# Kernel optimization log

Hardware: AMD Instinct MI355X
Metric: run time of the kernel (lower is better)

The kernel has to match this reference:

```python
import jax, jax.numpy as jnp
import numpy as np
import math

D_MODEL = 512
NUM_HEADS = 8
HEAD_DIM = D_MODEL // NUM_HEADS
B, L = 2, 2048
LN_EPS = 1e-5
DEN_EPS = 1e-5


def setup_inputs() -> dict:
    key = jax.random.key(0)
    ks = jax.random.split(key, 6)
    s = 1.0 / math.sqrt(D_MODEL)
    return {
        "x": jax.random.normal(ks[0], (B, L, D_MODEL), dtype=jnp.float32),
        "Wqkv": jax.random.normal(ks[1], (D_MODEL, 3 * D_MODEL), dtype=jnp.float32) * s,
        "bqkv": jnp.zeros((3 * D_MODEL,), dtype=jnp.float32),
        "Wout": jax.random.normal(ks[2], (D_MODEL, D_MODEL), dtype=jnp.float32) * s,
        "bout": jnp.zeros((D_MODEL,), dtype=jnp.float32),
        "ln_gamma": jnp.ones((D_MODEL,), dtype=jnp.float32),
        "ln_beta": jnp.zeros((D_MODEL,), dtype=jnp.float32),
        "decay_logits": jnp.full((NUM_HEADS,), 5.0, dtype=jnp.float32),
    }


def reference(x, Wqkv, bqkv, Wout, bout, ln_gamma, ln_beta, decay_logits):
    Bv, Lv, D = x.shape
    H = decay_logits.shape[0]
    E = D // H

    qkv = x @ Wqkv + bqkv                                   # [B,L,3D]
    q, k, v = jnp.split(qkv, 3, axis=-1)
    q = q.reshape(Bv, Lv, H, E)
    k = k.reshape(Bv, Lv, H, E)
    v = v.reshape(Bv, Lv, H, E)

    # ELU feature map + 1 -> positive features; scale q by 1/sqrt(E)
    q = (jax.nn.elu(q) + 1.0) / jnp.sqrt(jnp.asarray(E, x.dtype))
    k = jax.nn.elu(k) + 1.0

    lambdas = jax.nn.sigmoid(decay_logits).reshape(1, 1, H, 1)   # [1,1,H,1]
    t = jnp.arange(Lv, dtype=x.dtype).reshape(1, Lv, 1, 1)       # [1,L,1,1]
    decay_k = jnp.power(lambdas, -t)   # lambda^{-t}
    decay_q = jnp.power(lambdas, t)    # lambda^{t}

    k_dec = k * decay_k                                          # [B,L,H,E]
    kv = jnp.einsum('blhe,blhf->blhef', k_dec, v)                # [B,L,H,E,E]
    memory = jnp.cumsum(kv, axis=1)                              # prefix-sum scan over L
    k_sum = jnp.cumsum(k_dec, axis=1)                            # [B,L,H,E]

    q_dec = q * decay_q
    num = jnp.einsum('blhe,blhef->blhf', q_dec, memory)          # [B,L,H,E]
    den = jnp.einsum('blhe,blhe->blh', q_dec, k_sum)[..., None] + DEN_EPS
    out = (num / den).reshape(Bv, Lv, D)

    out = out @ Wout + bout

    # LayerNorm (eval mode; dropout is identity)
    mu = jnp.mean(out, axis=-1, keepdims=True)
    var = jnp.var(out, axis=-1, keepdims=True)
    out = (out - mu) / jnp.sqrt(var + LN_EPS) * ln_gamma + ln_beta
    return out
```

## Files before the change

kernel.cpp:

```cpp
#include <hip/hip_runtime.h>
#include <math.h>

#define B_ 2
#define L_ 2048
#define D_ 512
#define H_ 8
#define E_ 64
#define CHUNK 32
#define NCH 64
#define DEN_EPS_ 1e-5f
#define LN_EPS_ 1e-5f

typedef __bf16 bf16x8 __attribute__((ext_vector_type(8)));
typedef __bf16 bf16x4 __attribute__((ext_vector_type(4)));
typedef float  f32x4  __attribute__((ext_vector_type(4)));

__device__ __forceinline__ float sigm(float x) { return 1.f / (1.f + expf(-x)); }
__device__ __forceinline__ float elu1(float x) { return x > 0.f ? x + 1.f : expf(x); }

__global__ __launch_bounds__(256) void k_transpose_both(
    const float* __restrict__ W1, __bf16* __restrict__ D1,
    const float* __restrict__ W2, __bf16* __restrict__ D2)
{
    const float* src; __bf16* dst; int N;
    if (blockIdx.z == 0) { src = W1; dst = D1; N = 1536; }
    else                 { if (blockIdx.x >= 8) return; src = W2; dst = D2; N = 512; }
    const int K = 512;

    __shared__ __bf16 tile[64][68];
    const int kb = blockIdx.y * 64, nb = blockIdx.x * 64;
    const int t = threadIdx.x;
    const int rr = t >> 4, cc4 = (t & 15) * 4;
#pragma unroll
    for (int p = 0; p < 4; p++) {
        int k = rr + p * 16;
        float4 v = *(const float4*)&src[(size_t)(kb + k) * N + nb + cc4];
        tile[k][cc4 + 0] = (__bf16)v.x;
        tile[k][cc4 + 1] = (__bf16)v.y;
        tile[k][cc4 + 2] = (__bf16)v.z;
        tile[k][cc4 + 3] = (__bf16)v.w;
    }
    __syncthreads();
#pragma unroll
    for (int p = 0; p < 4; p++) {
        int n = rr + p * 16;
        bf16x4 o;
        o[0] = tile[cc4 + 0][n];
        o[1] = tile[cc4 + 1][n];
        o[2] = tile[cc4 + 2][n];
        o[3] = tile[cc4 + 3][n];
        *(bf16x4*)&dst[(size_t)(nb + n) * K + kb + cc4] = o;
    }
}

__global__ __launch_bounds__(256) void k_mfma_qkv(
    const float* __restrict__ X, const __bf16* __restrict__ Bt,
    const float* __restrict__ bias,
    __bf16* __restrict__ Qb, __bf16* __restrict__ Kb, __bf16* __restrict__ Vb)
{
    __shared__ __bf16 Al[128 * 32];
    __shared__ __bf16 Bl[128 * 32];
    const int t = threadIdx.x;
    const int w = t >> 6, lane = t & 63;
    const int wm = w >> 1, wn = w & 1;
    const int ll = lane & 15, quad = lane >> 4;
    const int m0 = blockIdx.y * 128, n0 = blockIdx.x * 128;

    f32x4 acc[4][4] = {};
    const int sr = t >> 2, sk = (t & 3) * 8;

    float4 pa0[2], pa1[2];
    bf16x8 pb[2];
    auto fetch = [&](int k0) {
#pragma unroll
        for (int h2 = 0; h2 < 2; h2++) {
            const float* ap = X + (size_t)(m0 + sr + h2 * 64) * D_ + k0 + sk;
            pa0[h2] = *(const float4*)ap;
            pa1[h2] = *(const float4*)(ap + 4);
        }
        pb[0] = *(const bf16x8*)&Bt[(size_t)(n0 + sr) * D_ + k0 + sk];
        pb[1] = *(const bf16x8*)&Bt[(size_t)(n0 + sr + 64) * D_ + k0 + sk];
    };

    fetch(0);
    for (int k0 = 0; k0 < D_; k0 += 32) {
#pragma unroll
        for (int h2 = 0; h2 < 2; h2++) {
            bf16x8 o;
            o[0] = (__bf16)pa0[h2].x; o[1] = (__bf16)pa0[h2].y;
            o[2] = (__bf16)pa0[h2].z; o[3] = (__bf16)pa0[h2].w;
            o[4] = (__bf16)pa1[h2].x; o[5] = (__bf16)pa1[h2].y;
            o[6] = (__bf16)pa1[h2].z; o[7] = (__bf16)pa1[h2].w;
            *(bf16x8*)&Al[(sr + h2 * 64) * 32 + sk] = o;
        }
        *(bf16x8*)&Bl[sr * 32 + sk]        = pb[0];
        *(bf16x8*)&Bl[(sr + 64) * 32 + sk] = pb[1];
        __syncthreads();
        if (k0 + 32 < D_) fetch(k0 + 32);
#pragma unroll
        for (int im = 0; im < 4; im++) {
            bf16x8 a = *(const bf16x8*)&Al[(wm * 64 + im * 16 + ll) * 32 + quad * 8];
#pragma unroll
            for (int in = 0; in < 4; in++) {
                bf16x8 b = *(const bf16x8*)&Bl[(wn * 64 + in * 16 + ll) * 32 + quad * 8];
                acc[im][in] = __builtin_amdgcn_mfma_f32_16x16x32_bf16(a, b, acc[im][in], 0, 0, 0);
            }
        }
        __syncthreads();
    }

    const int sec = n0 >> 9;
    __bf16* base = (sec == 0 ? Qb : (sec == 1 ? Kb : Vb));
#pragma unroll
    for (int im = 0; im < 4; im++) {
#pragma unroll
        for (int in = 0; in < 4; in++) {
            int n = n0 + wn * 64 + in * 16 + ll;
            int d = n & 511, h = d >> 6, e = d & 63;
            float bv = bias[n];
#pragma unroll
            for (int r = 0; r < 4; r++) {
                int m = m0 + wm * 64 + im * 16 + quad * 4 + r;
                int bb = m >> 11, l = m & 2047;
                float v = acc[im][in][r] + bv;
                if (sec == 0)      v = elu1(v) * 0.125f;
                else if (sec == 1) v = elu1(v);
                base[((size_t)((bb * H_ + h) * L_ + l)) * E_ + e] = (__bf16)v;
            }
        }
    }
}

__global__ __launch_bounds__(256) void k_chunk_g(
    const __bf16* __restrict__ Kb, const __bf16* __restrict__ Vb,
    const float* __restrict__ dl,
    __bf16* __restrict__ Gt, float* __restrict__ gn)
{
    __shared__ __bf16 Kwt[64][40];
    __shared__ __bf16 Vt[64][40];
    const int t  = threadIdx.x;
    const int bx = blockIdx.x;
    const int n = bx & 63, h = (bx >> 6) & 7, bb = bx >> 9;
    const int bh = bb * H_ + h;
    const float lam = sigm(dl[h]);

    {
        int i = t & 31, e0 = (t >> 5) * 8;
        size_t src = ((size_t)bh * L_ + n * CHUNK + i) * E_ + e0;
        float wk = powf(lam, (float)(CHUNK - 1 - i));
        bf16x8 k8 = *(const bf16x8*)&Kb[src];
        bf16x8 v8 = *(const bf16x8*)&Vb[src];
#pragma unroll
        for (int q = 0; q < 8; q++) {
            Kwt[e0 + q][i] = (__bf16)((float)k8[q] * wk);
            Vt[e0 + q][i]  = v8[q];
        }
    }
    __syncthreads();

    const int w = t >> 6, lane = t & 63;
    const int wm = w >> 1, wn = w & 1;
    const int ll = lane & 15, quad = lane >> 4;

    bf16x8 af[2], bf_[2];
#pragma unroll
    for (int a = 0; a < 2; a++) {
        af[a]  = *(const bf16x8*)&Vt[wm * 32 + a * 16 + ll][quad * 8];
        bf_[a] = *(const bf16x8*)&Kwt[wn * 32 + a * 16 + ll][quad * 8];
    }
    f32x4 acc[2][2] = {};
#pragma unroll
    for (int a = 0; a < 2; a++)
#pragma unroll
        for (int b = 0; b < 2; b++)
            acc[a][b] = __builtin_amdgcn_mfma_f32_16x16x32_bf16(af[a], bf_[b], acc[a][b], 0, 0, 0);

    size_t gbase = ((size_t)bh * NCH + n) * 4096;
#pragma unroll
    for (int a = 0; a < 2; a++)
#pragma unroll
        for (int b = 0; b < 2; b++)
#pragma unroll
            for (int r = 0; r < 4; r++) {
                int f = wm * 32 + a * 16 + quad * 4 + r;
                int e = wn * 32 + b * 16 + ll;
                Gt[gbase + (size_t)f * 64 + e] = (__bf16)acc[a][b][r];
            }

    if (t < 64) {
        float ga = 0.f;
#pragma unroll
        for (int k8 = 0; k8 < 4; k8++) {
            bf16x8 kk = *(const bf16x8*)&Kwt[t][k8 * 8];
#pragma unroll
            for (int q = 0; q < 8; q++) ga += (float)kk[q];
        }
        gn[((size_t)bh * NCH + n) * E_ + t] = ga;
    }
}

__global__ __launch_bounds__(64) void k_scan_par(
    const __bf16* __restrict__ Gt, const float* __restrict__ gn,
    const float* __restrict__ dl,
    __bf16* __restrict__ Sb, float* __restrict__ zl)
{
    const int lane = threadIdx.x;
    const int bh = blockIdx.x >> 6;
    const int j  = blockIdx.x & 63;
    const float lam = sigm(dl[bh & 7]);
    const float dC  = powf(lam, (float)CHUNK);

    const size_t base = ((size_t)bh * NCH) * 4096 + (size_t)j * 64 + lane;

    __bf16 g[NCH];
#pragma unroll
    for (int n = 0; n < NCH; n++) g[n] = Gt[base + (size_t)n * 4096];

    float s = 0.f;
#pragma unroll
    for (int n = 0; n < NCH; n++) {
        Sb[base + (size_t)n * 4096] = (__bf16)(lam * s);
        s = fmaf(dC, s, (float)g[n]);
    }

    float gv = gn[((size_t)bh * NCH + lane) * E_ + j];
    float wf = dC;
#pragma unroll
    for (int k = 1; k < 64; k <<= 1) {
        float up = __shfl_up(gv, k);
        if (lane >= k) gv = fmaf(wf, up, gv);
        wf = wf * wf;
    }
    float zex = __shfl_up(gv, 1);
    if (lane == 0) zex = 0.f;
    zl[((size_t)bh * NCH + lane) * E_ + j] = lam * zex;
}

__global__ __launch_bounds__(256) void k_attn(
    const __bf16* __restrict__ Qb, const __bf16* __restrict__ Kb,
    const __bf16* __restrict__ Vb,
    const __bf16* __restrict__ Sb, const float* __restrict__ zl,
    const float* __restrict__ dl, __bf16* __restrict__ Out)
{
    __shared__ __bf16 Qw[32][64];
    __shared__ __bf16 Kw[32][64];
    __shared__ __bf16 Vt[64][40];
    __shared__ __bf16 SbT[64][72];
    __shared__ __bf16 A1[32][40];
    __shared__ float  den[32];
    __shared__ float  zz[64];

    const int t  = threadIdx.x;
    const int bx = blockIdx.x;
    const int n = bx & 63, h = (bx >> 6) & 7, bb = bx >> 9;
    const int bh = bb * H_ + h;
    const float lam = sigm(dl[h]);

    {
        int i = t >> 3, e0 = (t & 7) * 8;
        size_t src = ((size_t)bh * L_ + n * CHUNK + i) * E_ + e0;
        float wq = powf(lam, (float)i);
        float wk = powf(lam, -(float)i);
        bf16x8 q8 = *(const bf16x8*)&Qb[src];
        bf16x8 k8 = *(const bf16x8*)&Kb[src];
        bf16x8 v8 = *(const bf16x8*)&Vb[src];
        bf16x8 qo, ko;
#pragma unroll
        for (int q = 0; q < 8; q++) {
            qo[q] = (__bf16)((float)q8[q] * wq);
            ko[q] = (__bf16)((float)k8[q] * wk);
            Vt[e0 + q][i] = v8[q];
        }
        *(bf16x8*)&Qw[i][e0] = qo;
        *(bf16x8*)&Kw[i][e0] = ko;

        int f = t >> 2, e00 = (t & 3) * 16;
        size_t sbase = ((size_t)bh * NCH + n) * 4096;
        bf16x8 s0 = *(const bf16x8*)&Sb[sbase + (size_t)f * 64 + e00];
        bf16x8 s1 = *(const bf16x8*)&Sb[sbase + (size_t)f * 64 + e00 + 8];
        *(bf16x8*)&SbT[f][e00]     = s0;
        *(bf16x8*)&SbT[f][e00 + 8] = s1;
        if (t < 64) zz[t] = zl[((size_t)bh * NCH + n) * E_ + t];
    }
    __syncthreads();

    const int w = t >> 6, lane = t & 63;
    const int ll = lane & 15, quad = lane >> 4;

    {
        const int wm = w >> 1, wn = w & 1;
        f32x4 accA = {};
#pragma unroll
        for (int ks = 0; ks < 2; ks++) {
            bf16x8 a = *(const bf16x8*)&Qw[wm * 16 + ll][ks * 32 + quad * 8];
            bf16x8 b = *(const bf16x8*)&Kw[wn * 16 + ll][ks * 32 + quad * 8];
            accA = __builtin_amdgcn_mfma_f32_16x16x32_bf16(a, b, accA, 0, 0, 0);
        }
        int j = wn * 16 + ll;
#pragma unroll
        for (int r = 0; r < 4; r++) {
            int i = wm * 16 + quad * 4 + r;
            A1[i][j] = (__bf16)(j <= i ? accA[r] : 0.f);
        }
    }
    __syncthreads();

    if (t < 32) {
        float rs = 0.f;
#pragma unroll
        for (int k8 = 0; k8 < 4; k8++) {
            bf16x8 aa = *(const bf16x8*)&A1[t][k8 * 8];
#pragma unroll
            for (int q = 0; q < 8; q++) rs += (float)aa[q];
        }
        float qz = 0.f;
#pragma unroll
        for (int e8 = 0; e8 < 8; e8++) {
            bf16x8 qq = *(const bf16x8*)&Qw[t][e8 * 8];
#pragma unroll
            for (int q = 0; q < 8; q++) qz += (float)qq[q] * zz[e8 * 8 + q];
        }
        den[t] = rs + qz + DEN_EPS_;
    }

    const int fw = w * 16;
    f32x4 acc1[2] = {}, acc2[2] = {};
    {
        bf16x8 bV = *(const bf16x8*)&Vt[fw + ll][quad * 8];
#pragma unroll
        for (int im = 0; im < 2; im++) {
            bf16x8 aA = *(const bf16x8*)&A1[im * 16 + ll][quad * 8];
            acc1[im] = __builtin_amdgcn_mfma_f32_16x16x32_bf16(aA, bV, acc1[im], 0, 0, 0);
        }
#pragma unroll
        for (int ks = 0; ks < 2; ks++) {
            bf16x8 bS = *(const bf16x8*)&SbT[fw + ll][ks * 32 + quad * 8];
#pragma unroll
            for (int im = 0; im < 2; im++) {
                bf16x8 aQ = *(const bf16x8*)&Qw[im * 16 + ll][ks * 32 + quad * 8];
                acc2[im] = __builtin_amdgcn_mfma_f32_16x16x32_bf16(aQ, bS, acc2[im], 0, 0, 0);
            }
        }
    }
    __syncthreads();

#pragma unroll
    for (int im = 0; im < 2; im++)
#pragma unroll
        for (int r = 0; r < 4; r++) {
            int i = im * 16 + quad * 4 + r;
            float o = (acc1[im][r] + acc2[im][r]) / den[i];
            Out[((size_t)bb * L_ + n * CHUNK + i) * D_ + h * E_ + fw + ll] = (__bf16)o;
        }
}

__global__ __launch_bounds__(256) void k_mfma_out_ln(
    const __bf16* __restrict__ Ab, const __bf16* __restrict__ Bt,
    const float* __restrict__ bias, const float* __restrict__ gam,
    const float* __restrict__ bet, float* __restrict__ Y)
{
    __shared__ __bf16 Al[32 * 32];
    __shared__ __bf16 Bl[512 * 32];
    __shared__ float gaml[512], betl[512], bl[512];
    __shared__ float redS[4][32], redQ[4][32];
    __shared__ float mv[32][2];

    const int t = threadIdx.x;
    const int w = t >> 6, lane = t & 63;
    const int ll = lane & 15, quad = lane >> 4;
    const int m0 = blockIdx.x * 32;

    {
        float2 g = *(const float2*)&gam[t * 2];
        float2 b2 = *(const float2*)&bet[t * 2];
        float2 bo = *(const float2*)&bias[t * 2];
        gaml[t * 2] = g.x;  gaml[t * 2 + 1] = g.y;
        betl[t * 2] = b2.x; betl[t * 2 + 1] = b2.y;
        bl[t * 2]   = bo.x; bl[t * 2 + 1]   = bo.y;
    }

    f32x4 acc[2][8] = {};
    const int sr = t >> 2, sk = (t & 3) * 8;

    bf16x8 pA;
    bf16x8 pB[8];
    auto fetch = [&](int k0) {
        if (t < 128)
            pA = *(const bf16x8*)&Ab[(size_t)(m0 + sr) * D_ + k0 + sk];
#pragma unroll
        for (int p = 0; p < 8; p++)
            pB[p] = *(const bf16x8*)&Bt[(size_t)(sr + p * 64) * D_ + k0 + sk];
    };

    fetch(0);
    for (int k0 = 0; k0 < D_; k0 += 32) {
        if (t < 128)
            *(bf16x8*)&Al[sr * 32 + sk] = pA;
#pragma unroll
        for (int p = 0; p < 8; p++)
            *(bf16x8*)&Bl[(sr + p * 64) * 32 + sk] = pB[p];
        __syncthreads();
        if (k0 + 32 < D_) fetch(k0 + 32);
#pragma unroll
        for (int im = 0; im < 2; im++) {
            bf16x8 a = *(const bf16x8*)&Al[(im * 16 + ll) * 32 + quad * 8];
#pragma unroll
            for (int in = 0; in < 8; in++) {
                bf16x8 b = *(const bf16x8*)&Bl[(w * 128 + in * 16 + ll) * 32 + quad * 8];
                acc[im][in] = __builtin_amdgcn_mfma_f32_16x16x32_bf16(a, b, acc[im][in], 0, 0, 0);
            }
        }
        __syncthreads();
    }

    float vals[2][8][4];
    float ps[2][4] = {}, pq[2][4] = {};
#pragma unroll
    for (int im = 0; im < 2; im++)
#pragma unroll
        for (int in = 0; in < 8; in++) {
            int col = w * 128 + in * 16 + ll;
            float bv = bl[col];
#pragma unroll
            for (int r = 0; r < 4; r++) {
                float v = acc[im][in][r] + bv;
                vals[im][in][r] = v;
                ps[im][r] += v;
                pq[im][r] += v * v;
            }
        }
#pragma unroll
    for (int im = 0; im < 2; im++)
#pragma unroll
        for (int r = 0; r < 4; r++) {
            float s = ps[im][r], q = pq[im][r];
            s += __shfl_xor(s, 1); q += __shfl_xor(q, 1);
            s += __shfl_xor(s, 2); q += __shfl_xor(q, 2);
            s += __shfl_xor(s, 4); q += __shfl_xor(q, 4);
            s += __shfl_xor(s, 8); q += __shfl_xor(q, 8);
            if (ll == 0) {
                int row = im * 16 + quad * 4 + r;
                redS[w][row] = s;
                redQ[w][row] = q;
            }
        }
    __syncthreads();
    if (t < 32) {
        float S = redS[0][t] + redS[1][t] + redS[2][t] + redS[3][t];
        float Q = redQ[0][t] + redQ[1][t] + redQ[2][t] + redQ[3][t];
        float mu  = S * (1.f / 512.f);
        float var = Q * (1.f / 512.f) - mu * mu;
        mv[t][0] = mu;
        mv[t][1] = rsqrtf(var + LN_EPS_);
    }
    __syncthreads();
#pragma unroll
    for (int im = 0; im < 2; im++)
#pragma unroll
        for (int r = 0; r < 4; r++) {
            int row = im * 16 + quad * 4 + r;
            float mu = mv[row][0], rs = mv[row][1];
#pragma unroll
            for (int in = 0; in < 8; in++) {
                int col = w * 128 + in * 16 + ll;
                Y[(size_t)(m0 + row) * D_ + col] =
                    (vals[im][in][r] - mu) * rs * gaml[col] + betl[col];
            }
        }
}

extern "C" void kernel_launch(void* const* d_in, const int* in_sizes, int n_in,
                              void* d_out, int out_size, void* d_ws, size_t ws_size,
                              hipStream_t stream)
{
    const float* x    = (const float*)d_in[0];
    const float* Wqkv = (const float*)d_in[1];
    const float* bqkv = (const float*)d_in[2];
    const float* Wout = (const float*)d_in[3];
    const float* bout = (const float*)d_in[4];
    const float* gam  = (const float*)d_in[5];
    const float* bet  = (const float*)d_in[6];
    const float* dl   = (const float*)d_in[7];
    float* out = (float*)d_out;

    const size_t NBHLE = (size_t)B_ * H_ * L_ * E_;
    const size_t NG    = (size_t)B_ * H_ * NCH * E_ * E_;
    const size_t Ng    = (size_t)B_ * H_ * NCH * E_;

    char* p = (char*)d_ws;
    __bf16* Gt  = (__bf16*)p;    p += NG * 2;
    __bf16* Sb  = (__bf16*)p;    p += NG * 2;
    float*  gn  = (float*)p;     p += Ng * 4;
    float*  zl  = (float*)p;     p += Ng * 4;
    __bf16* Qb  = (__bf16*)p;    p += NBHLE * 2;
    __bf16* Kb  = (__bf16*)p;    p += NBHLE * 2;
    __bf16* Vb  = (__bf16*)p;    p += NBHLE * 2;
    __bf16* WqkvT = (__bf16*)p;  p += (size_t)1536 * 512 * 2;
    __bf16* WoutT = (__bf16*)p;  p += (size_t)512 * 512 * 2;
    __bf16* Ao    = (__bf16*)p;  p += NBHLE * 2;

    dim3 blk(256);
    k_transpose_both<<<dim3(24, 8, 2), blk, 0, stream>>>(Wqkv, WqkvT, Wout, WoutT);
    k_mfma_qkv      <<<dim3(12, 32),   blk, 0, stream>>>(x, WqkvT, bqkv, Qb, Kb, Vb);
    k_chunk_g       <<<dim3(1024),     blk, 0, stream>>>(Kb, Vb, dl, Gt, gn);
    k_scan_par      <<<dim3(1024),     dim3(64), 0, stream>>>(Gt, gn, dl, Sb, zl);
    k_attn          <<<dim3(1024),     blk, 0, stream>>>(Qb, Kb, Vb, Sb, zl, dl, Ao);
    k_mfma_out_ln   <<<dim3(128),      blk, 0, stream>>>(Ao, WoutT, bout, gam, bet, out);
}
```

Measured before the change: 131.4 us.

## Use async global-to-LDS loads with swizzled LDS in GEMMs, pre-convert X to bf16

X is converted to bf16 in a prep kernel that also transposes the weights. Both GEMMs now stage tiles with global_load_lds direct copies into XOR-swizzled LDS instead of register prefetch plus ds_write. The attention kernel reads the state matrix straight into registers rather than through an LDS transpose, and swizzles the Q/K tiles to reduce bank conflicts. In exchange the GEMMs lose their register double-buffer prefetch, so load latency is no longer overlapped with MFMA work, and the X conversion costs an extra pass over memory.

```diff
diff --git a/kernel.cpp b/kernel.cpp
--- a/kernel.cpp
+++ b/kernel.cpp
@@ -18,18 +18,41 @@
 __device__ __forceinline__ float sigm(float x) { return 1.f / (1.f + expf(-x)); }
 __device__ __forceinline__ float elu1(float x) { return x > 0.f ? x + 1.f : expf(x); }
 
-__global__ __launch_bounds__(256) void k_transpose_both(
+__device__ __forceinline__ void async_cp16(const void* g, void* l) {
+    __builtin_amdgcn_global_load_lds(
+        (const __attribute__((address_space(1))) void*)g,
+        (__attribute__((address_space(3))) void*)l, 16, 0, 0);
+}
+
+#define SWZ4(row, q) ((((q) ^ ((row) & 3)) * 8))
+
+__global__ __launch_bounds__(256) void k_prep(
     const float* __restrict__ W1, __bf16* __restrict__ D1,
-    const float* __restrict__ W2, __bf16* __restrict__ D2)
-{
+    const float* __restrict__ W2, __bf16* __restrict__ D2,
+    const float* __restrict__ X,  __bf16* __restrict__ Xb)
+{
+    const int t = threadIdx.x;
+    if (blockIdx.z == 2) {
+        int id = ((int)blockIdx.y * 32 + (int)blockIdx.x) * 256 + t;
+#pragma unroll
+        for (int it = 0; it < 4; it++) {
+            size_t i = (size_t)it * 524288 + (size_t)id * 8;
+            float4 a = *(const float4*)&X[i];
+            float4 b = *(const float4*)&X[i + 4];
+            bf16x8 o;
+            o[0] = (__bf16)a.x; o[1] = (__bf16)a.y; o[2] = (__bf16)a.z; o[3] = (__bf16)a.w;
+            o[4] = (__bf16)b.x; o[5] = (__bf16)b.y; o[6] = (__bf16)b.z; o[7] = (__bf16)b.w;
+            *(bf16x8*)&Xb[i] = o;
+        }
+        return;
+    }
     const float* src; __bf16* dst; int N;
-    if (blockIdx.z == 0) { src = W1; dst = D1; N = 1536; }
-    else                 { if (blockIdx.x >= 8) return; src = W2; dst = D2; N = 512; }
+    if (blockIdx.z == 0) { if (blockIdx.x >= 24) return; src = W1; dst = D1; N = 1536; }
+    else                 { if (blockIdx.x >= 8)  return; src = W2; dst = D2; N = 512; }
     const int K = 512;
 
     __shared__ __bf16 tile[64][68];
     const int kb = blockIdx.y * 64, nb = blockIdx.x * 64;
-    const int t = threadIdx.x;
     const int rr = t >> 4, cc4 = (t & 15) * 4;
 #pragma unroll
     for (int p = 0; p < 4; p++) {
@@ -54,7 +77,7 @@
 }
 
 __global__ __launch_bounds__(256) void k_mfma_qkv(
-    const float* __restrict__ X, const __bf16* __restrict__ Bt,
+    const __bf16* __restrict__ Ab, const __bf16* __restrict__ Bt,
     const float* __restrict__ bias,
     __bf16* __restrict__ Qb, __bf16* __restrict__ Kb, __bf16* __restrict__ Vb)
 {
@@ -67,42 +90,28 @@
     const int m0 = blockIdx.y * 128, n0 = blockIdx.x * 128;
 
     f32x4 acc[4][4] = {};
-    const int sr = t >> 2, sk = (t & 3) * 8;
-
-    float4 pa0[2], pa1[2];
-    bf16x8 pb[2];
-    auto fetch = [&](int k0) {
-#pragma unroll
-        for (int h2 = 0; h2 < 2; h2++) {
-            const float* ap = X + (size_t)(m0 + sr + h2 * 64) * D_ + k0 + sk;
-            pa0[h2] = *(const float4*)ap;
-            pa1[h2] = *(const float4*)(ap + 4);
-        }
-        pb[0] = *(const bf16x8*)&Bt[(size_t)(n0 + sr) * D_ + k0 + sk];
-        pb[1] = *(const bf16x8*)&Bt[(size_t)(n0 + sr + 64) * D_ + k0 + sk];
-    };
-
-    fetch(0);
+    const int sr  = t >> 2;
+    const int skz = (((t & 3) ^ (sr & 3)) * 8);
+
+    __bf16* A0 = &Al[(w * 16) * 32];
+    __bf16* A1p = &Al[(64 + w * 16) * 32];
+    __bf16* B0 = &Bl[(w * 16) * 32];
+    __bf16* B1p = &Bl[(64 + w * 16) * 32];
+
     for (int k0 = 0; k0 < D_; k0 += 32) {
-#pragma unroll
-        for (int h2 = 0; h2 < 2; h2++) {
-            bf16x8 o;
-            o[0] = (__bf16)pa0[h2].x; o[1] = (__bf16)pa0[h2].y;
-            o[2] = (__bf16)pa0[h2].z; o[3] = (__bf16)pa0[h2].w;
-            o[4] = (__bf16)pa1[h2].x; o[5] = (__bf16)pa1[h2].y;
-            o[6] = (__bf16)pa1[h2].z; o[7] = (__bf16)pa1[h2].w;
-            *(bf16x8*)&Al[(sr + h2 * 64) * 32 + sk] = o;
-        }
-        *(bf16x8*)&Bl[sr * 32 + sk]        = pb[0];
-        *(bf16x8*)&Bl[(sr + 64) * 32 + sk] = pb[1];
+        async_cp16(&Ab[(size_t)(m0 + sr) * D_ + k0 + skz],      A0);
+        async_cp16(&Ab[(size_t)(m0 + 64 + sr) * D_ + k0 + skz], A1p);
+        async_cp16(&Bt[(size_t)(n0 + sr) * D_ + k0 + skz],      B0);
+        async_cp16(&Bt[(size_t)(n0 + 64 + sr) * D_ + k0 + skz], B1p);
         __syncthreads();
-        if (k0 + 32 < D_) fetch(k0 + 32);
 #pragma unroll
         for (int im = 0; im < 4; im++) {
-            bf16x8 a = *(const bf16x8*)&Al[(wm * 64 + im * 16 + ll) * 32 + quad * 8];
+            int ra = wm * 64 + im * 16 + ll;
+            bf16x8 a = *(const bf16x8*)&Al[ra * 32 + SWZ4(ra, quad)];
 #pragma unroll
             for (int in = 0; in < 4; in++) {
-                bf16x8 b = *(const bf16x8*)&Bl[(wn * 64 + in * 16 + ll) * 32 + quad * 8];
+                int rb = wn * 64 + in * 16 + ll;
+                bf16x8 b = *(const bf16x8*)&Bl[rb * 32 + SWZ4(rb, quad)];
                 acc[im][in] = __builtin_amdgcn_mfma_f32_16x16x32_bf16(a, b, acc[im][in], 0, 0, 0);
             }
         }
@@ -245,7 +254,6 @@
     __shared__ __bf16 Qw[32][64];
     __shared__ __bf16 Kw[32][64];
     __shared__ __bf16 Vt[64][40];
-    __shared__ __bf16 SbT[64][72];
     __shared__ __bf16 A1[32][40];
     __shared__ float  den[32];
     __shared__ float  zz[64];
@@ -256,44 +264,45 @@
     const int bh = bb * H_ + h;
     const float lam = sigm(dl[h]);
 
+    const int w = t >> 6, lane = t & 63;
+    const int ll = lane & 15, quad = lane >> 4;
+    const int fw = w * 16;
+    const size_t sbase = ((size_t)bh * NCH + n) * 4096;
+
+    bf16x8 bS0 = *(const bf16x8*)&Sb[sbase + (size_t)(fw + ll) * 64 + quad * 8];
+    bf16x8 bS1 = *(const bf16x8*)&Sb[sbase + (size_t)(fw + ll) * 64 + 32 + quad * 8];
+
     {
-        int i = t >> 3, e0 = (t & 7) * 8;
-        size_t src = ((size_t)bh * L_ + n * CHUNK + i) * E_ + e0;
+        int i = t >> 3, e0c = t & 7;
+        size_t src = ((size_t)bh * L_ + n * CHUNK + i) * E_ + e0c * 8;
         float wq = powf(lam, (float)i);
         float wk = powf(lam, -(float)i);
         bf16x8 q8 = *(const bf16x8*)&Qb[src];
         bf16x8 k8 = *(const bf16x8*)&Kb[src];
         bf16x8 v8 = *(const bf16x8*)&Vb[src];
         bf16x8 qo, ko;
+        int e0 = e0c * 8;
 #pragma unroll
         for (int q = 0; q < 8; q++) {
             qo[q] = (__bf16)((float)q8[q] * wq);
             ko[q] = (__bf16)((float)k8[q] * wk);
             Vt[e0 + q][i] = v8[q];
         }
-        *(bf16x8*)&Qw[i][e0] = qo;
-        *(bf16x8*)&Kw[i][e0] = ko;
-
-        int f = t >> 2, e00 = (t & 3) * 16;
-        size_t sbase = ((size_t)bh * NCH + n) * 4096;
-        bf16x8 s0 = *(const bf16x8*)&Sb[sbase + (size_t)f * 64 + e00];
-        bf16x8 s1 = *(const bf16x8*)&Sb[sbase + (size_t)f * 64 + e00 + 8];
-        *(bf16x8*)&SbT[f][e00]     = s0;
-        *(bf16x8*)&SbT[f][e00 + 8] = s1;
+        int cs = (e0c ^ (i & 7)) * 8;
+        *(bf16x8*)&Qw[i][cs] = qo;
+        *(bf16x8*)&Kw[i][cs] = ko;
         if (t < 64) zz[t] = zl[((size_t)bh * NCH + n) * E_ + t];
     }
     __syncthreads();
-
-    const int w = t >> 6, lane = t & 63;
-    const int ll = lane & 15, quad = lane >> 4;
 
     {
         const int wm = w >> 1, wn = w & 1;
+        int ra = wm * 16 + ll, rb = wn * 16 + ll;
         f32x4 accA = {};
 #pragma unroll
         for (int ks = 0; ks < 2; ks++) {
-            bf16x8 a = *(const bf16x8*)&Qw[wm * 16 + ll][ks * 32 + quad * 8];
-            bf16x8 b = *(const bf16x8*)&Kw[wn * 16 + ll][ks * 32 + quad * 8];
+            bf16x8 a = *(const bf16x8*)&Qw[ra][((ks * 4 + quad) ^ (ra & 7)) * 8];
+            bf16x8 b = *(const bf16x8*)&Kw[rb][((ks * 4 + quad) ^ (rb & 7)) * 8];
             accA = __builtin_amdgcn_mfma_f32_16x16x32_bf16(a, b, accA, 0, 0, 0);
         }
         int j = wn * 16 + ll;
@@ -316,14 +325,13 @@
         float qz = 0.f;
 #pragma unroll
         for (int e8 = 0; e8 < 8; e8++) {
-            bf16x8 qq = *(const bf16x8*)&Qw[t][e8 * 8];
-#pragma unroll
-            for (int q = 0; q < 8; q++) qz += (float)qq[q] * zz[e8 * 8 + q];
+            bf16x8 qq = *(const bf16x8*)&Qw[t][(e8 ^ (t & 7)) * 8];
+#pragma unroll
+            for (int q = 0; q < 8; q++) qz += (float)qq[q] * zz[(e8 ^ (t & 7)) * 8 + q];
         }
         den[t] = rs + qz + DEN_EPS_;
     }
 
-    const int fw = w * 16;
     f32x4 acc1[2] = {}, acc2[2] = {};
     {
         bf16x8 bV = *(const bf16x8*)&Vt[fw + ll][quad * 8];
@@ -333,13 +341,12 @@
             acc1[im] = __builtin_amdgcn_mfma_f32_16x16x32_bf16(aA, bV, acc1[im], 0, 0, 0);
         }
 #pragma unroll
-        for (int ks = 0; ks < 2; ks++) {
-            bf16x8 bS = *(const bf16x8*)&SbT[fw + ll][ks * 32 + quad * 8];
-#pragma unroll
-            for (int im = 0; im < 2; im++) {
-                bf16x8 aQ = *(const bf16x8*)&Qw[im * 16 + ll][ks * 32 + quad * 8];
-                acc2[im] = __builtin_amdgcn_mfma_f32_16x16x32_bf16(aQ, bS, acc2[im], 0, 0, 0);
-            }
+        for (int im = 0; im < 2; im++) {
+            int ra = im * 16 + ll;
+            bf16x8 aQ0 = *(const bf16x8*)&Qw[ra][((quad) ^ (ra & 7)) * 8];
+            bf16x8 aQ1 = *(const bf16x8*)&Qw[ra][((4 + quad) ^ (ra & 7)) * 8];
+            acc2[im] = __builtin_amdgcn_mfma_f32_16x16x32_bf16(aQ0, bS0, acc2[im], 0, 0, 0);
+            acc2[im] = __builtin_amdgcn_mfma_f32_16x16x32_bf16(aQ1, bS1, acc2[im], 0, 0, 0);
         }
     }
     __syncthreads();
@@ -380,33 +387,25 @@
     }
 
     f32x4 acc[2][8] = {};
-    const int sr = t >> 2, sk = (t & 3) * 8;
-
-    bf16x8 pA;
-    bf16x8 pB[8];
-    auto fetch = [&](int k0) {
-        if (t < 128)
-            pA = *(const bf16x8*)&Ab[(size_t)(m0 + sr) * D_ + k0 + sk];
-#pragma unroll
-        for (int p = 0; p < 8; p++)
-            pB[p] = *(const bf16x8*)&Bt[(size_t)(sr + p * 64) * D_ + k0 + sk];
-    };
-
-    fetch(0);
+    const int sr  = t >> 2;
+    const int skz = (((t & 3) ^ (sr & 3)) * 8);
+    __bf16* Ald = &Al[(w * 16) * 32];
+
     for (int k0 = 0; k0 < D_; k0 += 32) {
         if (t < 128)
-            *(bf16x8*)&Al[sr * 32 + sk] = pA;
+            async_cp16(&Ab[(size_t)(m0 + sr) * D_ + k0 + skz], Ald);
 #pragma unroll
         for (int p = 0; p < 8; p++)
-            *(bf16x8*)&Bl[(sr + p * 64) * 32 + sk] = pB[p];
+            async_cp16(&Bt[(size_t)(p * 64 + sr) * D_ + k0 + skz], &Bl[(p * 64 + w * 16) * 32]);
         __syncthreads();
-        if (k0 + 32 < D_) fetch(k0 + 32);
 #pragma unroll
         for (int im = 0; im < 2; im++) {
-            bf16x8 a = *(const bf16x8*)&Al[(im * 16 + ll) * 32 + quad * 8];
+            int ra = im * 16 + ll;
+            bf16x8 a = *(const bf16x8*)&Al[ra * 32 + SWZ4(ra, quad)];
 #pragma unroll
             for (int in = 0; in < 8; in++) {
-                bf16x8 b = *(const bf16x8*)&Bl[(w * 128 + in * 16 + ll) * 32 + quad * 8];
+                int rb = w * 128 + in * 16 + ll;
+                bf16x8 b = *(const bf16x8*)&Bl[rb * 32 + SWZ4(rb, quad)];
                 acc[im][in] = __builtin_amdgcn_mfma_f32_16x16x32_bf16(a, b, acc[im][in], 0, 0, 0);
             }
         }
@@ -495,15 +494,16 @@
     __bf16* Qb  = (__bf16*)p;    p += NBHLE * 2;
     __bf16* Kb  = (__bf16*)p;    p += NBHLE * 2;
     __bf16* Vb  = (__bf16*)p;    p += NBHLE * 2;
+    __bf16* Xb    = (__bf16*)p;  p += NBHLE * 2;
     __bf16* WqkvT = (__bf16*)p;  p += (size_t)1536 * 512 * 2;
     __bf16* WoutT = (__bf16*)p;  p += (size_t)512 * 512 * 2;
     __bf16* Ao    = (__bf16*)p;  p += NBHLE * 2;
 
     dim3 blk(256);
-    k_transpose_both<<<dim3(24, 8, 2), blk, 0, stream>>>(Wqkv, WqkvT, Wout, WoutT);
-    k_mfma_qkv      <<<dim3(12, 32),   blk, 0, stream>>>(x, WqkvT, bqkv, Qb, Kb, Vb);
-    k_chunk_g       <<<dim3(1024),     blk, 0, stream>>>(Kb, Vb, dl, Gt, gn);
-    k_scan_par      <<<dim3(1024),     dim3(64), 0, stream>>>(Gt, gn, dl, Sb, zl);
-    k_attn          <<<dim3(1024),     blk, 0, stream>>>(Qb, Kb, Vb, Sb, zl, dl, Ao);
-    k_mfma_out_ln   <<<dim3(128),      blk, 0, stream>>>(Ao, WoutT, bout, gam, bet, out);
-}
+    k_prep        <<<dim3(32, 8, 3), blk, 0, stream>>>(Wqkv, WqkvT, Wout, WoutT, x, Xb);
+    k_mfma_qkv    <<<dim3(12, 32),   blk, 0, stream>>>(Xb, WqkvT, bqkv, Qb, Kb, Vb);
+    k_chunk_g     <<<dim3(1024),     blk, 0, stream>>>(Kb, Vb, dl, Gt, gn);
+    k_scan_par    <<<dim3(1024),     dim3(64), 0, stream>>>(Gt, gn, dl, Sb, zl);
+    k_attn        <<<dim3(1024),     blk, 0, stream>>>(Qb, Kb, Vb, Sb, zl, dl, Ao);
+    k_mfma_out_ln <<<dim3(128),      blk, 0, stream>>>(Ao, WoutT, bout, gam, bet, out);
+}
```

Measured after the change: 133.4 us. About the same (+1.6%).
